# Performance work log

Hardware: AMD Instinct MI355X
Metric: run time of the kernel (lower is better)

The kernel has to match this reference:

```python
import jax, jax.numpy as jnp
import numpy as np

KERNEL_SIZE = 5
GROUP_SIZE = 1
SCALE = 2


def setup_inputs() -> dict:
    key = jax.random.key(0)
    k1, k2 = jax.random.split(key)
    N, C, H, W = 2, 256, 128, 128
    features = jax.random.normal(k1, (N, C, H, W), dtype=jnp.float32)
    masks = jax.random.uniform(
        k2, (N, KERNEL_SIZE * KERNEL_SIZE * GROUP_SIZE, H * SCALE, W * SCALE),
        dtype=jnp.float32)
    return {"features": features, "masks": masks}


def reference(features, masks):
    # CARAFE: content-aware reassembly upsampling.
    # out[n,c,i,j] = sum_{dy,dx} feat[n,c, i//s + dy - r, j//s + dx - r]
    #                * masks[n, g*K*K + dy*K + dx, i, j]
    K, G, s = KERNEL_SIZE, GROUP_SIZE, SCALE
    N, C, H, W = features.shape
    Cg = C // G
    K2 = K * K
    r = K // 2
    # zero-pad spatially and gather all K*K shifted views -> (N, C, K2, H, W)
    fp = jnp.pad(features, ((0, 0), (0, 0), (r, r), (r, r)))
    patches = jnp.stack(
        [fp[:, :, dy:dy + H, dx:dx + W] for dy in range(K) for dx in range(K)],
        axis=2)
    patches = patches.reshape(N, G, Cg, K2, H, W)
    # masks at output resolution; split each output pixel into (src_pixel, subpixel)
    m = masks.reshape(N, G, K2, H, s, W, s)
    # weighted reduce over the kernel window, broadcast over channels in group
    out = jnp.einsum('ngckhw,ngkhawb->ngchawb', patches, m)
    return out.reshape(N, C, H * s, W * s)
```

## Files before the change

### kernel.cpp

```cpp
#include <hip/hip_runtime.h>

#define KK 5
#define RR 2
#define N_ 2
#define C_ 256
#define H_ 128
#define W_ 128
#define H2 256
#define W2 256
#define TH 16
#define TW 16
#define CCHUNK 16
#define PH 20
#define PW 20
#define PHPW 400
#define HW (H_*W_)
#define HW2 (H2*W2)
#define DEPTH 4

__global__ __launch_bounds__(256) void carafe_kernel(
    const float* __restrict__ feat,
    const float* __restrict__ masks,
    float* __restrict__ out)
{
    __shared__ float patch[4 * PHPW * 4];

    const int tid = threadIdx.x;
    const int tx = tid & 15;
    const int ty = tid >> 4;
    const int bx = blockIdx.x & 7;
    const int by = blockIdx.x >> 3;
    const int c0 = blockIdx.y * CCHUNK;
    const int n  = blockIdx.z;

    const int i0 = by * TH + ty;
    const int j0 = bx * TW + tx;
    const int gy0 = by * TH - RR;
    const int gx0 = bx * TW - RR;

    const float* mb = masks + ((size_t)n * (KK * KK) * H2 + (size_t)(2 * i0)) * W2 + 2 * j0;
    float2 q0[DEPTH], q1[DEPTH];
    #pragma unroll
    for (int t = 0; t < DEPTH; ++t) {
        q0[t] = *reinterpret_cast<const float2*>(mb + (size_t)t * HW2);
        q1[t] = *reinterpret_cast<const float2*>(mb + (size_t)t * HW2 + W2);
    }

    const float* fbase = feat + (size_t)(n * C_ + c0) * HW;
    #pragma unroll
    for (int r = 0; r < 7; ++r) {
        const int idx = tid + r * 256;
        if (idx < 4 * PHPW) {
            const int G  = idx / PHPW;
            const int p  = idx - G * PHPW;
            const int py = p / PW;
            const int px = p - py * PW;
            const int gy = gy0 + py;
            const int gx = gx0 + px;
            float4 v = make_float4(0.f, 0.f, 0.f, 0.f);
            if ((unsigned)gy < (unsigned)H_ && (unsigned)gx < (unsigned)W_) {
                const float* fp = fbase + (4 * G) * HW + gy * W_ + gx;
                v.x = fp[0];
                v.y = fp[HW];
                v.z = fp[2 * HW];
                v.w = fp[3 * HW];
            }
            *reinterpret_cast<float4*>(&patch[G * 1600 + p * 4]) = v;
        }
    }
    __syncthreads();

    float acc[CCHUNK][2][2] = {};
    const int p0 = ty * PW + tx;

    #pragma unroll
    for (int k = 0; k < KK * KK; ++k) {
        const float2 m0 = q0[k % DEPTH];
        const float2 m1 = q1[k % DEPTH];
        if (k + DEPTH < KK * KK) {
            q0[k % DEPTH] = *reinterpret_cast<const float2*>(mb + (size_t)(k + DEPTH) * HW2);
            q1[k % DEPTH] = *reinterpret_cast<const float2*>(mb + (size_t)(k + DEPTH) * HW2 + W2);
        }
        const int dy = k / KK;
        const int dx = k - KK * dy;
        const int P  = p0 + dy * PW + dx;
        const float4 v0 = *reinterpret_cast<const float4*>(&patch[P * 4]);
        const float4 v1 = *reinterpret_cast<const float4*>(&patch[1600 + P * 4]);
        const float4 v2 = *reinterpret_cast<const float4*>(&patch[3200 + P * 4]);
        const float4 v3 = *reinterpret_cast<const float4*>(&patch[4800 + P * 4]);
        const float va[16] = { v0.x, v0.y, v0.z, v0.w,  v1.x, v1.y, v1.z, v1.w,
                               v2.x, v2.y, v2.z, v2.w,  v3.x, v3.y, v3.z, v3.w };
        #pragma unroll
        for (int c = 0; c < 16; ++c) {
            acc[c][0][0] += va[c] * m0.x;  acc[c][0][1] += va[c] * m0.y;
            acc[c][1][0] += va[c] * m1.x;  acc[c][1][1] += va[c] * m1.y;
        }
    }

    #pragma unroll
    for (int c = 0; c < CCHUNK; ++c) {
        float* ob = out + ((size_t)(n * C_ + c0 + c) * H2 + (size_t)(2 * i0)) * W2 + 2 * j0;
        *reinterpret_cast<float2*>(ob)      = make_float2(acc[c][0][0], acc[c][0][1]);
        *reinterpret_cast<float2*>(ob + W2) = make_float2(acc[c][1][0], acc[c][1][1]);
    }
}

extern "C" void kernel_launch(void* const* d_in, const int* in_sizes, int n_in,
                              void* d_out, int out_size, void* d_ws, size_t ws_size,
                              hipStream_t stream) {
    const float* feat  = (const float*)d_in[0];
    const float* masks = (const float*)d_in[1];
    float* out = (float*)d_out;

    dim3 grid((W_ / TW) * (H_ / TH),
              C_ / CCHUNK,
              N_);
    carafe_kernel<<<grid, dim3(256), 0, stream>>>(feat, masks, out);
}
```

Before: 53.51 us.

## Remap threads to two pixels by four channels with sliding-window LDS reuse

Each thread now computes two horizontally adjacent source pixels for four channels, and the block's two thread halves split an 8-channel chunk, halving CCHUNK and doubling the grid. For each kernel row a thread loads a 6-wide window of LDS values once and reuses it across the 5 dx taps. Mask loads and output stores widen to float4. The LDS row stride is padded to 21 to reduce bank conflicts. The aim is fewer LDS reads per FMA, smaller shared memory and more blocks. The cost is that each mask element is now read by twice as many blocks in total.

```diff
diff --git a/kernel.cpp b/kernel.cpp
--- a/kernel.cpp
+++ b/kernel.cpp
@@ -10,53 +10,48 @@
 #define W2 256
 #define TH 16
 #define TW 16
-#define CCHUNK 16
+#define CCHUNK 8
 #define PH 20
-#define PW 20
-#define PHPW 400
+#define PWPIX 20
+#define PSTR 21
+#define PLANE (PH*PSTR*4)
 #define HW (H_*W_)
 #define HW2 (H2*W2)
-#define DEPTH 4
+#define DEPTH 2
 
 __global__ __launch_bounds__(256) void carafe_kernel(
     const float* __restrict__ feat,
     const float* __restrict__ masks,
     float* __restrict__ out)
 {
-    __shared__ float patch[4 * PHPW * 4];
+    __shared__ float patch[2 * PLANE];
 
     const int tid = threadIdx.x;
-    const int tx = tid & 15;
-    const int ty = tid >> 4;
-    const int bx = blockIdx.x & 7;
-    const int by = blockIdx.x >> 3;
-    const int c0 = blockIdx.y * CCHUNK;
-    const int n  = blockIdx.z;
+    const int q   = tid >> 7;
+    const int pp  = tid & 127;
+    const int txp = pp & 7;
+    const int ty  = pp >> 3;
+    const int bx  = blockIdx.x & 7;
+    const int by  = blockIdx.x >> 3;
+    const int c0  = blockIdx.y * CCHUNK;
+    const int n   = blockIdx.z;
 
     const int i0 = by * TH + ty;
-    const int j0 = bx * TW + tx;
+    const int j0 = bx * TW + 2 * txp;
     const int gy0 = by * TH - RR;
     const int gx0 = bx * TW - RR;
 
-    const float* mb = masks + ((size_t)n * (KK * KK) * H2 + (size_t)(2 * i0)) * W2 + 2 * j0;
-    float2 q0[DEPTH], q1[DEPTH];
-    #pragma unroll
-    for (int t = 0; t < DEPTH; ++t) {
-        q0[t] = *reinterpret_cast<const float2*>(mb + (size_t)t * HW2);
-        q1[t] = *reinterpret_cast<const float2*>(mb + (size_t)t * HW2 + W2);
-    }
-
     const float* fbase = feat + (size_t)(n * C_ + c0) * HW;
     #pragma unroll
-    for (int r = 0; r < 7; ++r) {
+    for (int r = 0; r < 4; ++r) {
         const int idx = tid + r * 256;
-        if (idx < 4 * PHPW) {
-            const int G  = idx / PHPW;
-            const int p  = idx - G * PHPW;
-            const int py = p / PW;
-            const int px = p - py * PW;
-            const int gy = gy0 + py;
-            const int gx = gx0 + px;
+        if (idx < 2 * PH * PWPIX) {
+            const int G   = idx >= PH * PWPIX;
+            const int pix = idx - G * (PH * PWPIX);
+            const int py  = pix / PWPIX;
+            const int px  = pix - py * PWPIX;
+            const int gy  = gy0 + py;
+            const int gx  = gx0 + px;
             float4 v = make_float4(0.f, 0.f, 0.f, 0.f);
             if ((unsigned)gy < (unsigned)H_ && (unsigned)gx < (unsigned)W_) {
                 const float* fp = fbase + (4 * G) * HW + gy * W_ + gx;
@@ -65,43 +60,60 @@
                 v.z = fp[2 * HW];
                 v.w = fp[3 * HW];
             }
-            *reinterpret_cast<float4*>(&patch[G * 1600 + p * 4]) = v;
+            *reinterpret_cast<float4*>(&patch[G * PLANE + (py * PSTR + px) * 4]) = v;
         }
+    }
+
+    const float* mb = masks + ((size_t)n * (KK * KK) * H2 + (size_t)(2 * i0)) * W2 + 2 * j0;
+    float4 qr[DEPTH][2];
+    #pragma unroll
+    for (int t = 0; t < DEPTH; ++t) {
+        qr[t][0] = *reinterpret_cast<const float4*>(mb + (size_t)t * HW2);
+        qr[t][1] = *reinterpret_cast<const float4*>(mb + (size_t)t * HW2 + W2);
     }
     __syncthreads();
 
-    float acc[CCHUNK][2][2] = {};
-    const int p0 = ty * PW + tx;
+    float acc[4][2][2][2] = {};
+    const int rb0 = q * PLANE + (ty * PSTR + 2 * txp) * 4;
 
     #pragma unroll
-    for (int k = 0; k < KK * KK; ++k) {
-        const float2 m0 = q0[k % DEPTH];
-        const float2 m1 = q1[k % DEPTH];
-        if (k + DEPTH < KK * KK) {
-            q0[k % DEPTH] = *reinterpret_cast<const float2*>(mb + (size_t)(k + DEPTH) * HW2);
-            q1[k % DEPTH] = *reinterpret_cast<const float2*>(mb + (size_t)(k + DEPTH) * HW2 + W2);
-        }
-        const int dy = k / KK;
-        const int dx = k - KK * dy;
-        const int P  = p0 + dy * PW + dx;
-        const float4 v0 = *reinterpret_cast<const float4*>(&patch[P * 4]);
-        const float4 v1 = *reinterpret_cast<const float4*>(&patch[1600 + P * 4]);
-        const float4 v2 = *reinterpret_cast<const float4*>(&patch[3200 + P * 4]);
-        const float4 v3 = *reinterpret_cast<const float4*>(&patch[4800 + P * 4]);
-        const float va[16] = { v0.x, v0.y, v0.z, v0.w,  v1.x, v1.y, v1.z, v1.w,
-                               v2.x, v2.y, v2.z, v2.w,  v3.x, v3.y, v3.z, v3.w };
+    for (int dy = 0; dy < KK; ++dy) {
+        float4 w[6];
         #pragma unroll
-        for (int c = 0; c < 16; ++c) {
-            acc[c][0][0] += va[c] * m0.x;  acc[c][0][1] += va[c] * m0.y;
-            acc[c][1][0] += va[c] * m1.x;  acc[c][1][1] += va[c] * m1.y;
+        for (int u = 0; u < 6; ++u)
+            w[u] = *reinterpret_cast<const float4*>(&patch[rb0 + dy * (PSTR * 4) + u * 4]);
+
+        #pragma unroll
+        for (int dx = 0; dx < KK; ++dx) {
+            const int k = dy * KK + dx;
+            const float4 m0 = qr[k % DEPTH][0];
+            const float4 m1 = qr[k % DEPTH][1];
+            if (k + DEPTH < KK * KK) {
+                qr[k % DEPTH][0] = *reinterpret_cast<const float4*>(mb + (size_t)(k + DEPTH) * HW2);
+                qr[k % DEPTH][1] = *reinterpret_cast<const float4*>(mb + (size_t)(k + DEPTH) * HW2 + W2);
+            }
+            const float4 w0 = w[dx];
+            const float4 w1 = w[dx + 1];
+            const float wa0[4] = { w0.x, w0.y, w0.z, w0.w };
+            const float wa1[4] = { w1.x, w1.y, w1.z, w1.w };
+            #pragma unroll
+            for (int t = 0; t < 4; ++t) {
+                acc[t][0][0][0] += wa0[t] * m0.x;  acc[t][0][0][1] += wa0[t] * m0.y;
+                acc[t][1][0][0] += wa1[t] * m0.z;  acc[t][1][0][1] += wa1[t] * m0.w;
+                acc[t][0][1][0] += wa0[t] * m1.x;  acc[t][0][1][1] += wa0[t] * m1.y;
+                acc[t][1][1][0] += wa1[t] * m1.z;  acc[t][1][1][1] += wa1[t] * m1.w;
+            }
         }
     }
 
     #pragma unroll
-    for (int c = 0; c < CCHUNK; ++c) {
-        float* ob = out + ((size_t)(n * C_ + c0 + c) * H2 + (size_t)(2 * i0)) * W2 + 2 * j0;
-        *reinterpret_cast<float2*>(ob)      = make_float2(acc[c][0][0], acc[c][0][1]);
-        *reinterpret_cast<float2*>(ob + W2) = make_float2(acc[c][1][0], acc[c][1][1]);
+    for (int t = 0; t < 4; ++t) {
+        #pragma unroll
+        for (int a = 0; a < 2; ++a) {
+            float* ob = out + ((size_t)(n * C_ + c0 + 4 * q + t) * H2 + (size_t)(2 * i0 + a)) * W2 + 2 * j0;
+            *reinterpret_cast<float4*>(ob) =
+                make_float4(acc[t][0][a][0], acc[t][0][a][1], acc[t][1][a][0], acc[t][1][a][1]);
+        }
     }
 }
 
```

New measurement: 57.77 us. +8.0%, slower.
